# Optimization experiments

Hardware: AMD Instinct MI355X
Metric: run time of the kernel (lower is better)

The kernel has to match this reference:

```python
import jax, jax.numpy as jnp
import numpy as np
import math

N, K, M = 4, 3, 3
OUTC, INC = 64, 64

def _valid_combos():
    combos = []
    for n in range(1, N + 1):
        for k in range(K):
            for m in range(-M, M + 1):
                if abs(m) <= k and k < n:
                    combos.append((n, k, m))
    return combos

COMBOS = _valid_combos()  # 23 (n,k,m) triples, static


def _assoc_laguerre(k, a, x):
    # L_k^a(x) = sum_{i=0}^k (-1)^i C(k+a, k-i) x^i / i!  (static small degree)
    out = jnp.zeros_like(x)
    for i in range(k + 1):
        c = ((-1) ** i) * math.comb(k + a, k - i) / math.factorial(i)
        out = out + jnp.asarray(c, x.dtype) * x ** i
    return out


def _assoc_legendre(l, m, ct, st):
    # P_l^m(cos t) with Condon-Shortley phase; ct=cos t, st=sin t >= 0
    if m > 0:
        dfact = math.prod(range(1, 2 * m, 2))  # (2m-1)!!
        pmm = jnp.asarray(((-1) ** m) * dfact, ct.dtype) * st ** m
    else:
        pmm = jnp.ones_like(ct)
    if l == m:
        return pmm
    pmmp1 = ct * (2 * m + 1) * pmm
    if l == m + 1:
        return pmmp1
    for ll in range(m + 2, l + 1):
        pll = ((2 * ll - 1) * ct * pmmp1 - (ll + m - 1) * pmm) / (ll - m)
        pmm, pmmp1 = pmmp1, pll
    return pmmp1


def _hwfr(n, l, m, r, ct, st, phi):
    # real hydrogen-like wavefunction psi_{n,l,m}(r,theta,phi), a0 = 1
    rho = 2.0 * r / n
    norm_r = math.sqrt((2.0 / n) ** 3 * math.factorial(n - l - 1) / (2 * n * math.factorial(n + l)))
    R = norm_r * jnp.exp(-0.5 * rho) * rho ** l * _assoc_laguerre(n - l - 1, 2 * l + 1, rho)
    am = abs(m)
    Klm = math.sqrt((2 * l + 1) / (4 * math.pi) * math.factorial(l - am) / math.factorial(l + am))
    P = _assoc_legendre(l, am, ct, st)
    if m > 0:
        Y = math.sqrt(2.0) * Klm * jnp.cos(am * phi) * P
    elif m < 0:
        Y = math.sqrt(2.0) * Klm * jnp.sin(am * phi) * P
    else:
        Y = Klm * P
    return R * Y


def setup_inputs() -> dict:
    key = jax.random.key(0)
    k1, k2 = jax.random.split(key)
    position = jax.random.normal(k1, (8, 4096, 3), dtype=jnp.float32)
    coefficients = jax.random.normal(k2, (OUTC, INC, len(COMBOS)), dtype=jnp.float32)
    return {"position": position, "coefficients": coefficients}


def reference(position, coefficients):
    x, y, z = position[..., 0], position[..., 1], position[..., 2]
    r = jnp.sqrt(x * x + y * y + z * z) + 1e-12
    ct = z / r
    st = jnp.sqrt(jnp.clip(1.0 - ct * ct, 0.0, None))
    phi = jnp.arctan2(y, x)
    # (B, P, n_basis) -- loop over the small static basis set, not data dims
    poly = jnp.stack([_hwfr(n, l, m, r, ct, st, phi) for (n, l, m) in COMBOS], axis=-1)
    # einsum 'ijk, mnk -> mnij' as in the torch module -> (OutC, InC, B, P)
    return jnp.einsum('ijk,mnk->mnij', poly, coefficients)
```

## Files before the change

kernel.cpp:

```cpp
#include <hip/hip_runtime.h>
#include <hip/hip_bf16.h>
#include <math.h>

#define NPTS  32768
#define NPAIR 4096
#define NC    23
#define PSPLIT 16
#define PPB   (NPAIR / PSPLIT)
#define TPB   256

namespace cgen {
constexpr double PI = 3.14159265358979323846264338327950288;
constexpr double fact(int n) { double r = 1; for (int i = 2; i <= n; ++i) r *= i; return r; }
constexpr double comb(int n, int k) { double r = 1; for (int i = 0; i < k; ++i) r = r * (n - i) / (i + 1); return r; }
constexpr double csqrt(double x) { double g = x > 1 ? x : 1.0; for (int i = 0; i < 100; ++i) g = 0.5 * (g + x / g); return g; }

struct Tables {
  int n[NC]; int l[NC]; int m[NC];
  double pref[NC];
  double lag[NC][4];
};
constexpr Tables gen() {
  Tables t{};
  int idx = 0;
  for (int n = 1; n <= 4; ++n)
    for (int k = 0; k < 3; ++k)
      for (int m = -3; m <= 3; ++m) {
        int am = m < 0 ? -m : m;
        if (!(am <= k && k < n)) continue;
        t.n[idx] = n; t.l[idx] = k; t.m[idx] = m;
        double norm_r = csqrt((2.0 / n) * (2.0 / n) * (2.0 / n) * fact(n - k - 1) / (2.0 * n * fact(n + k)));
        double Klm = csqrt((2.0 * k + 1.0) / (4.0 * PI) * fact(k - am) / fact(k + am));
        t.pref[idx] = norm_r * Klm * (m != 0 ? csqrt(2.0) : 1.0);
        int kk = n - k - 1, a = 2 * k + 1;
        for (int i = 0; i < 4; ++i) t.lag[idx][i] = 0.0;
        for (int i = 0; i <= kk; ++i)
          t.lag[idx][i] = ((i & 1) ? -1.0 : 1.0) * comb(kk + a, kk - i) / fact(i);
        ++idx;
      }
  return t;
}
constexpr Tables T = gen();
}

__global__ __launch_bounds__(TPB)
void dcconv_poly_einsum(const float* __restrict__ pos,
                        const float* __restrict__ coef,
                        float* __restrict__ out) {
  const int pt    = blockIdx.x * TPB + threadIdx.x;
  const int pair0 = blockIdx.y * PPB;

  const float x = pos[3 * pt + 0];
  const float y = pos[3 * pt + 1];
  const float z = pos[3 * pt + 2];

  const float r   = sqrtf(x * x + y * y + z * z) + 1e-12f;
  const float ct  = z / r;
  const float st2 = fmaxf(1.0f - ct * ct, 0.0f);
  const float st  = sqrtf(st2);
  const float phi = atan2f(y, x);
  float sp, cp;
  sincosf(phi, &sp, &cp);
  const float c2p = cp * cp - sp * sp;
  const float s2p = 2.0f * sp * cp;

  float rho[5]; rho[0] = 0.0f; rho[1] = 2.0f * r; rho[2] = r; rho[3] = (2.0f / 3.0f) * r; rho[4] = 0.5f * r;
  float en[5];  en[0] = 0.0f;
  en[1] = expf(-r); en[2] = expf(-0.5f * r); en[3] = expf(-(1.0f / 3.0f) * r); en[4] = expf(-0.25f * r);

  float P[3][3] = {};
  P[0][0] = 1.0f;
  P[1][0] = ct;                    P[1][1] = -st;
  P[2][0] = 1.5f * ct * ct - 0.5f; P[2][1] = -3.0f * ct * st; P[2][2] = 3.0f * st2;

  float trig[5]; trig[0] = s2p; trig[1] = sp; trig[2] = 1.0f; trig[3] = cp; trig[4] = c2p;

  float poly[NC];
#pragma unroll
  for (int c = 0; c < NC; ++c) {
    const int n = cgen::T.n[c], l = cgen::T.l[c], m = cgen::T.m[c];
    const int am = m < 0 ? -m : m;
    const float rh = rho[n];
    const float L = (float)cgen::T.lag[c][0]
                  + rh * ((float)cgen::T.lag[c][1]
                  + rh * ((float)cgen::T.lag[c][2]
                  + rh *  (float)cgen::T.lag[c][3]));
    const float rl = (l == 0) ? 1.0f : ((l == 1) ? rh : rh * rh);
    poly[c] = (float)cgen::T.pref[c] * en[n] * rl * L * P[l][am] * trig[m + 2];
  }

  const float* __restrict__ cptr = coef + (size_t)pair0 * NC;
  float* __restrict__ optr = out + (size_t)pair0 * NPTS + pt;
#pragma unroll 4
  for (int j = 0; j < PPB; ++j) {
    float acc = 0.0f;
#pragma unroll
    for (int c = 0; c < NC; ++c) acc = fmaf(cptr[c], poly[c], acc);
    *optr = acc;
    cptr += NC;
    optr += NPTS;
  }
}

extern "C" void kernel_launch(void* const* d_in, const int* in_sizes, int n_in,
                              void* d_out, int out_size, void* d_ws, size_t ws_size,
                              hipStream_t stream) {
  const float* pos  = (const float*)d_in[0];
  const float* coef = (const float*)d_in[1];
  float* out = (float*)d_out;

  dim3 grid(NPTS / TPB, PSPLIT);
  dim3 block(TPB);
  hipLaunchKernelGGL(dcconv_poly_einsum, grid, block, 0, stream, pos, coef, out);
}
```

Measured before the change: 667.0 us.

## Stage coefficient tiles in LDS and compute four points per thread with float4 stores

Each block now loads a 64-pair slice of the coefficient matrix into shared memory, padded to 24 floats per row for float4 reads. Each thread evaluates the basis for four consecutive points and writes float4 outputs. This is meant to cut scalar global coefficient loads and widen the output stores. In exchange, the basis is recomputed for more pair tiles and register pressure rises from holding four basis vectors.

```diff
diff --git a/kernel.cpp b/kernel.cpp
--- a/kernel.cpp
+++ b/kernel.cpp
@@ -1,13 +1,14 @@
 #include <hip/hip_runtime.h>
-#include <hip/hip_bf16.h>
 #include <math.h>
 
 #define NPTS  32768
 #define NPAIR 4096
 #define NC    23
-#define PSPLIT 16
-#define PPB   (NPAIR / PSPLIT)
 #define TPB   256
+#define PPT   4
+#define PTS_PER_BLOCK (TPB * PPT)
+#define PT    64
+#define NCP   24
 
 namespace cgen {
 constexpr double PI = 3.14159265358979323846264338327950288;
@@ -47,59 +48,106 @@
 void dcconv_poly_einsum(const float* __restrict__ pos,
                         const float* __restrict__ coef,
                         float* __restrict__ out) {
-  const int pt    = blockIdx.x * TPB + threadIdx.x;
-  const int pair0 = blockIdx.y * PPB;
+  __shared__ __align__(16) float lc[PT * NCP];
 
-  const float x = pos[3 * pt + 0];
-  const float y = pos[3 * pt + 1];
-  const float z = pos[3 * pt + 2];
+  const int tid   = threadIdx.x;
+  const int pt0   = blockIdx.x * PTS_PER_BLOCK + tid * PPT;
+  const int pair0 = blockIdx.y * PT;
 
-  const float r   = sqrtf(x * x + y * y + z * z) + 1e-12f;
-  const float ct  = z / r;
-  const float st2 = fmaxf(1.0f - ct * ct, 0.0f);
-  const float st  = sqrtf(st2);
-  const float phi = atan2f(y, x);
-  float sp, cp;
-  sincosf(phi, &sp, &cp);
-  const float c2p = cp * cp - sp * sp;
-  const float s2p = 2.0f * sp * cp;
-
-  float rho[5]; rho[0] = 0.0f; rho[1] = 2.0f * r; rho[2] = r; rho[3] = (2.0f / 3.0f) * r; rho[4] = 0.5f * r;
-  float en[5];  en[0] = 0.0f;
-  en[1] = expf(-r); en[2] = expf(-0.5f * r); en[3] = expf(-(1.0f / 3.0f) * r); en[4] = expf(-0.25f * r);
-
-  float P[3][3] = {};
-  P[0][0] = 1.0f;
-  P[1][0] = ct;                    P[1][1] = -st;
-  P[2][0] = 1.5f * ct * ct - 0.5f; P[2][1] = -3.0f * ct * st; P[2][2] = 3.0f * st2;
-
-  float trig[5]; trig[0] = s2p; trig[1] = sp; trig[2] = 1.0f; trig[3] = cp; trig[4] = c2p;
-
-  float poly[NC];
+  {
+    const float* __restrict__ cb = coef + (size_t)pair0 * NC;
 #pragma unroll
-  for (int c = 0; c < NC; ++c) {
-    const int n = cgen::T.n[c], l = cgen::T.l[c], m = cgen::T.m[c];
-    const int am = m < 0 ? -m : m;
-    const float rh = rho[n];
-    const float L = (float)cgen::T.lag[c][0]
-                  + rh * ((float)cgen::T.lag[c][1]
-                  + rh * ((float)cgen::T.lag[c][2]
-                  + rh *  (float)cgen::T.lag[c][3]));
-    const float rl = (l == 0) ? 1.0f : ((l == 1) ? rh : rh * rh);
-    poly[c] = (float)cgen::T.pref[c] * en[n] * rl * L * P[l][am] * trig[m + 2];
+    for (int i = tid; i < PT * NC; i += TPB) {
+      const int row = i / NC;
+      const int col = i - row * NC;
+      lc[row * NCP + col] = cb[i];
+    }
+    if (tid < PT) lc[tid * NCP + NC] = 0.0f;
   }
 
-  const float* __restrict__ cptr = coef + (size_t)pair0 * NC;
-  float* __restrict__ optr = out + (size_t)pair0 * NPTS + pt;
-#pragma unroll 4
-  for (int j = 0; j < PPB; ++j) {
-    float acc = 0.0f;
+  const float4* __restrict__ pv = reinterpret_cast<const float4*>(pos + (size_t)pt0 * 3);
+  const float4 q0 = pv[0], q1 = pv[1], q2 = pv[2];
+
+  float p0[NC], p1[NC], p2[NC], p3[NC];
+
+  auto evalpt = [&](float x, float y, float z, float (&pc)[NC]) {
+    const float r   = sqrtf(x * x + y * y + z * z) + 1e-12f;
+    const float ct  = z / r;
+    const float st2 = fmaxf(1.0f - ct * ct, 0.0f);
+    const float st  = sqrtf(st2);
+    const float phi = atan2f(y, x);
+    float sp, cp;
+    sincosf(phi, &sp, &cp);
+    const float c2p = cp * cp - sp * sp;
+    const float s2p = 2.0f * sp * cp;
+
+    float rho[5]; rho[0] = 0.0f; rho[1] = 2.0f * r; rho[2] = r; rho[3] = (2.0f / 3.0f) * r; rho[4] = 0.5f * r;
+    float en[5];  en[0] = 0.0f;
+    en[1] = expf(-r); en[2] = expf(-0.5f * r); en[3] = expf(-(1.0f / 3.0f) * r); en[4] = expf(-0.25f * r);
+
+    float P[3][3] = {};
+    P[0][0] = 1.0f;
+    P[1][0] = ct;                    P[1][1] = -st;
+    P[2][0] = 1.5f * ct * ct - 0.5f; P[2][1] = -3.0f * ct * st; P[2][2] = 3.0f * st2;
+
+    float trig[5]; trig[0] = s2p; trig[1] = sp; trig[2] = 1.0f; trig[3] = cp; trig[4] = c2p;
+
 #pragma unroll
-    for (int c = 0; c < NC; ++c) acc = fmaf(cptr[c], poly[c], acc);
-    *optr = acc;
-    cptr += NC;
+    for (int c = 0; c < NC; ++c) {
+      const int n = cgen::T.n[c], l = cgen::T.l[c], m = cgen::T.m[c];
+      const int am = m < 0 ? -m : m;
+      const float rh = rho[n];
+      const float L = (float)cgen::T.lag[c][0]
+                    + rh * ((float)cgen::T.lag[c][1]
+                    + rh * ((float)cgen::T.lag[c][2]
+                    + rh *  (float)cgen::T.lag[c][3]));
+      const float rl = (l == 0) ? 1.0f : ((l == 1) ? rh : rh * rh);
+      pc[c] = (float)cgen::T.pref[c] * en[n] * rl * L * P[l][am] * trig[m + 2];
+    }
+  };
+
+  evalpt(q0.x, q0.y, q0.z, p0);
+  evalpt(q0.w, q1.x, q1.y, p1);
+  evalpt(q1.z, q1.w, q2.x, p2);
+  evalpt(q2.y, q2.z, q2.w, p3);
+
+  __syncthreads();
+
+  const float4* __restrict__ lrow = reinterpret_cast<const float4*>(lc);
+  float* __restrict__ optr = out + (size_t)pair0 * NPTS + pt0;
+
+#define G4(CV, B)                                                                      \
+  a0 = fmaf(CV.x, p0[(B)+0], a0); a1 = fmaf(CV.x, p1[(B)+0], a1);                       \
+  a2 = fmaf(CV.x, p2[(B)+0], a2); a3 = fmaf(CV.x, p3[(B)+0], a3);                       \
+  a0 = fmaf(CV.y, p0[(B)+1], a0); a1 = fmaf(CV.y, p1[(B)+1], a1);                       \
+  a2 = fmaf(CV.y, p2[(B)+1], a2); a3 = fmaf(CV.y, p3[(B)+1], a3);                       \
+  a0 = fmaf(CV.z, p0[(B)+2], a0); a1 = fmaf(CV.z, p1[(B)+2], a1);                       \
+  a2 = fmaf(CV.z, p2[(B)+2], a2); a3 = fmaf(CV.z, p3[(B)+2], a3);                       \
+  a0 = fmaf(CV.w, p0[(B)+3], a0); a1 = fmaf(CV.w, p1[(B)+3], a1);                       \
+  a2 = fmaf(CV.w, p2[(B)+3], a2); a3 = fmaf(CV.w, p3[(B)+3], a3);
+
+#define G3(CV, B)                                                                      \
+  a0 = fmaf(CV.x, p0[(B)+0], a0); a1 = fmaf(CV.x, p1[(B)+0], a1);                       \
+  a2 = fmaf(CV.x, p2[(B)+0], a2); a3 = fmaf(CV.x, p3[(B)+0], a3);                       \
+  a0 = fmaf(CV.y, p0[(B)+1], a0); a1 = fmaf(CV.y, p1[(B)+1], a1);                       \
+  a2 = fmaf(CV.y, p2[(B)+1], a2); a3 = fmaf(CV.y, p3[(B)+1], a3);                       \
+  a0 = fmaf(CV.z, p0[(B)+2], a0); a1 = fmaf(CV.z, p1[(B)+2], a1);                       \
+  a2 = fmaf(CV.z, p2[(B)+2], a2); a3 = fmaf(CV.z, p3[(B)+2], a3);
+
+#pragma unroll 2
+  for (int j = 0; j < PT; ++j) {
+    const float4 c0 = lrow[0], c1 = lrow[1], c2 = lrow[2],
+                 c3 = lrow[3], c4 = lrow[4], c5 = lrow[5];
+    lrow += 6;
+
+    float a0 = 0.0f, a1 = 0.0f, a2 = 0.0f, a3 = 0.0f;
+    G4(c0, 0) G4(c1, 4) G4(c2, 8) G4(c3, 12) G4(c4, 16) G3(c5, 20)
+
+    *reinterpret_cast<float4*>(optr) = make_float4(a0, a1, a2, a3);
     optr += NPTS;
   }
+#undef G4
+#undef G3
 }
 
 extern "C" void kernel_launch(void* const* d_in, const int* in_sizes, int n_in,
@@ -109,7 +157,7 @@
   const float* coef = (const float*)d_in[1];
   float* out = (float*)d_out;
 
-  dim3 grid(NPTS / TPB, PSPLIT);
+  dim3 grid(NPTS / PTS_PER_BLOCK, NPAIR / PT);
   dim3 block(TPB);
   hipLaunchKernelGGL(dcconv_poly_einsum, grid, block, 0, stream, pos, coef, out);
 }
```

New measurement: 546.7 us. -18.0%, faster.
